# Kernel tuning notes

Hardware: AMD Instinct MI355X
Metric: run time of the kernel (lower is better)

Reference implementation:

```python
import jax, jax.numpy as jnp
import numpy as np

B, FIXED_LEN, N_FRAME, MID, P = 4096, 8192, 2112, 264, 88
UNROLLED_ITER = 5


def setup_inputs() -> dict:
    key = jax.random.key(0)
    ks = jax.random.split(key, 8)
    # Fourier weights scaled by 1/FIXED_LEN as in fourier_init
    W_cos = jax.random.normal(ks[0], (N_FRAME, FIXED_LEN), jnp.float32) / FIXED_LEN
    W_sin = jax.random.normal(ks[1], (N_FRAME, FIXED_LEN), jnp.float32) / FIXED_LEN
    # template is |cisoid_dict|^2 >= 0; small positive values keep the unrolled loop stable
    template = jax.random.uniform(ks[2], (N_FRAME, MID), jnp.float32) * 0.01
    return {
        "input_this": jax.random.normal(ks[3], (B, FIXED_LEN), jnp.float32),
        "input_prev": jax.random.normal(ks[4], (B, FIXED_LEN), jnp.float32),
        "W_cos": W_cos,
        "W_sin": W_sin,
        "template": template,
        "W1": jax.random.normal(ks[5], (MID, MID), jnp.float32) * 0.05 + jnp.eye(MID, dtype=jnp.float32),
        "b1": jnp.zeros((MID,), jnp.float32),
        "W2": jax.random.normal(ks[6], (P, MID), jnp.float32) * 0.1,
        "b2": jnp.zeros((P,), jnp.float32),
        "Wout": jax.random.normal(ks[7], (P, P), jnp.float32) * 0.1 + 4.0 * jnp.eye(P, dtype=jnp.float32),
        "bout": jnp.full((P,), -3.0, jnp.float32),
    }


def reference(input_this, input_prev, W_cos, W_sin, template, W1, b1, W2, b2, Wout, bout):
    fixed_len = jnp.asarray(input_this.shape[1], input_this.dtype)
    # get_feat: normalized power spectrum features
    n_valid = (jnp.count_nonzero(input_this, axis=1) + 1).astype(input_this.dtype)[:, None]
    scale = fixed_len / n_valid                      # [B, 1]
    x_cos = (input_this @ W_cos.T) * scale           # [B, N_FRAME]
    x_sin = (input_this @ W_sin.T) * scale
    feat = x_cos * x_cos + x_sin * x_sin             # [B, N_FRAME]

    # process_feat: unrolled LISTA-style iterations
    running = feat
    xi = -running
    m = jax.nn.relu(-10.0 * (xi @ template))         # [B, MID]
    for _ in range(UNROLLED_ITER - 1):
        xi = 1.6 * ((m @ template.T) - running) + 0.2 * xi
        m = jax.nn.relu(-8.0 * (xi @ template) + 0.2 * m)

    h = jax.nn.relu(jax.nn.relu(m @ W1.T + b1) @ W2.T + b2)  # [B, P]
    return jax.nn.sigmoid(h @ Wout.T + bout)         # velocity_estimate [B, P]
```

## Files before the change

kernel.cpp:

```cpp
#include <hip/hip_runtime.h>
#include <cstdint>
#include <cstddef>

#define B_SZ 4096
#define KLEN 8192
#define NF   2112
#define MID  264
#define PD   88

typedef _Float16 f16;
typedef _Float16 f16x4 __attribute__((ext_vector_type(4)));
typedef _Float16 f16x8 __attribute__((ext_vector_type(8)));
typedef float    f32x4 __attribute__((ext_vector_type(4)));

__device__ __forceinline__ void gl2lds16(const void* g, void* l) {
    __builtin_amdgcn_global_load_lds(
        (const __attribute__((address_space(1))) void*)g,
        (__attribute__((address_space(3))) void*)l, 16, 0, 0);
}

__global__ void k_row_prep(const float* __restrict__ x, f16* __restrict__ xh,
                           float* __restrict__ alpha) {
    const int row = blockIdx.x;
    const float* xr = x + (size_t)row * KLEN;
    f16* xhr = xh + (size_t)row * KLEN;
    int cnt = 0;
    for (int j = threadIdx.x * 4; j < KLEN; j += 256 * 4) {
        float4 v = *(const float4*)(xr + j);
        f16x4 h = { (f16)v.x, (f16)v.y, (f16)v.z, (f16)v.w };
        *(f16x4*)(xhr + j) = h;
        cnt += (v.x != 0.f) + (v.y != 0.f) + (v.z != 0.f) + (v.w != 0.f);
    }
    for (int off = 32; off > 0; off >>= 1) cnt += __shfl_down(cnt, off);
    __shared__ int lsum[4];
    if ((threadIdx.x & 63) == 0) lsum[threadIdx.x >> 6] = cnt;
    __syncthreads();
    if (threadIdx.x == 0)
        alpha[row] = 8.0f / (float)(lsum[0] + lsum[1] + lsum[2] + lsum[3] + 1);
}

__global__ void k_cvt_w2(const float* __restrict__ wc, const float* __restrict__ ws,
                         f16* __restrict__ whc, f16* __restrict__ whs, int n4) {
    const float* w = blockIdx.y ? ws : wc;
    f16* wh = blockIdx.y ? whs : whc;
    for (int i = blockIdx.x * blockDim.x + threadIdx.x; i < n4; i += gridDim.x * blockDim.x) {
        float4 v = ((const float4*)w)[i];
        f16x4 h = { (f16)(v.x * 8192.f), (f16)(v.y * 8192.f),
                    (f16)(v.z * 8192.f), (f16)(v.w * 8192.f) };
        ((f16x4*)wh)[i] = h;
    }
}

__global__ void k_prep_tt(const float* __restrict__ T, f16* __restrict__ tt) {
    __shared__ float tile[32][33];
    const int k0 = blockIdx.x * 32, n0 = blockIdx.y * 32;
    const int tx = threadIdx.x & 31, ty = threadIdx.x >> 5;
    for (int r = ty; r < 32; r += 8) {
        const int k = k0 + r, n = n0 + tx;
        tile[r][tx] = (n < MID) ? T[(size_t)k * MID + n] : 0.f;
    }
    __syncthreads();
    for (int r = ty; r < 32; r += 8) {
        const int n = n0 + r, k = k0 + tx;
        tt[(size_t)n * NF + k] = (f16)tile[tx][r];
    }
}

__global__ void k_gram(const float* __restrict__ T, float* __restrict__ G) {
    __shared__ float Pp[32][64];
    __shared__ float Qq[32][64];
    const int i0 = blockIdx.x * 64, j0 = blockIdx.y * 64;
    const int tx = threadIdx.x & 15, ty = threadIdx.x >> 4;
    float acc[4][4] = {};
    for (int kc = blockIdx.z * 11; kc < (int)blockIdx.z * 11 + 11; ++kc) {
        const int k0 = kc * 32;
        for (int l = threadIdx.x; l < 32 * 64; l += 256) {
            const int kk = l >> 6, cc = l & 63, kr = k0 + kk;
            Pp[kk][cc] = (i0 + cc < MID) ? T[(size_t)kr * MID + i0 + cc] : 0.f;
            Qq[kk][cc] = (j0 + cc < MID) ? T[(size_t)kr * MID + j0 + cc] : 0.f;
        }
        __syncthreads();
        for (int kk = 0; kk < 32; ++kk) {
            float a_[4], b_[4];
#pragma unroll
            for (int u = 0; u < 4; ++u) a_[u] = Pp[kk][tx * 4 + u];
#pragma unroll
            for (int w = 0; w < 4; ++w) b_[w] = Qq[kk][ty * 4 + w];
#pragma unroll
            for (int u = 0; u < 4; ++u)
#pragma unroll
                for (int w = 0; w < 4; ++w) acc[u][w] += a_[u] * b_[w];
        }
        __syncthreads();
    }
    for (int u = 0; u < 4; ++u) {
        const int gi = i0 + tx * 4 + u;
        if (gi >= MID) continue;
        for (int w = 0; w < 4; ++w) {
            const int gj = j0 + ty * 4 + w;
            if (gj < MID) atomicAdd(&G[(size_t)gi * MID + gj], acc[u][w]);
        }
    }
}

__global__ __launch_bounds__(256, 4) void k_fourier(
    const f16* __restrict__ A, const f16* __restrict__ Bc, const f16* __restrict__ Bs,
    const float* __restrict__ alpha, f16* __restrict__ feat) {
    __shared__ __align__(16) f16 As[128 * 64];
    __shared__ __align__(16) f16 Bcs[64 * 64];
    __shared__ __align__(16) f16 Bss[64 * 64];
    const int tid = threadIdx.x, lane = tid & 63, wave = tid >> 6;
    const int wm = wave & 1, wn = wave >> 1;

    const int bid = blockIdx.y * 33 + blockIdx.x;
    const int swz = (bid & 7) * 132 + (bid >> 3);
    const int bx = swz % 33, by = swz / 33;
    const int m0 = by * 128, n0 = bx * 64;

    const int srow = tid >> 3;
    const int scol = ((tid & 7) ^ (srow & 7)) << 3;
    const f16* gA  = A  + (size_t)(m0 + srow) * KLEN + scol;
    const f16* gBc = Bc + (size_t)(n0 + srow) * KLEN + scol;
    const f16* gBs = Bs + (size_t)(n0 + srow) * KLEN + scol;

#define STAGE_F(kq)                                                               \
    {                                                                             \
        _Pragma("unroll")                                                         \
        for (int i = 0; i < 4; ++i)                                               \
            gl2lds16(gA + (size_t)(32 * i) * KLEN + (kq),                         \
                     (char*)&As[0] + (tid + 256 * i) * 16);                       \
        _Pragma("unroll")                                                         \
        for (int i = 0; i < 2; ++i)                                               \
            gl2lds16(gBc + (size_t)(32 * i) * KLEN + (kq),                        \
                     (char*)&Bcs[0] + (tid + 256 * i) * 16);                      \
        _Pragma("unroll")                                                         \
        for (int i = 0; i < 2; ++i)                                               \
            gl2lds16(gBs + (size_t)(32 * i) * KLEN + (kq),                        \
                     (char*)&Bss[0] + (tid + 256 * i) * 16);                      \
    }

    f32x4 accC[4][2], accS[4][2];
    const f32x4 z4 = {0.f, 0.f, 0.f, 0.f};
#pragma unroll
    for (int i = 0; i < 4; ++i)
#pragma unroll
        for (int j = 0; j < 2; ++j) { accC[i][j] = z4; accS[i][j] = z4; }

    for (int k0 = 0; k0 < KLEN; k0 += 64) {
        if (k0) __syncthreads();
        STAGE_F(k0);
        __syncthreads();
#pragma unroll
        for (int kk = 0; kk < 2; ++kk) {
            const int chunk0 = kk * 4 + (lane >> 4);
            f16x8 af[4], bcf[2], bsf[2];
#pragma unroll
            for (int mt = 0; mt < 4; ++mt) {
                const int r = wm * 64 + mt * 16 + (lane & 15);
                af[mt] = *(const f16x8*)(&As[0] + r * 64 + ((chunk0 ^ (r & 7)) << 3));
            }
#pragma unroll
            for (int nt = 0; nt < 2; ++nt) {
                const int r = wn * 32 + nt * 16 + (lane & 15);
                const int off = r * 64 + ((chunk0 ^ (r & 7)) << 3);
                bcf[nt] = *(const f16x8*)(&Bcs[0] + off);
                bsf[nt] = *(const f16x8*)(&Bss[0] + off);
            }
#pragma unroll
            for (int mt = 0; mt < 4; ++mt)
#pragma unroll
                for (int nt = 0; nt < 2; ++nt) {
                    accC[mt][nt] = __builtin_amdgcn_mfma_f32_16x16x32_f16(af[mt], bcf[nt], accC[mt][nt], 0, 0, 0);
                    accS[mt][nt] = __builtin_amdgcn_mfma_f32_16x16x32_f16(af[mt], bsf[nt], accS[mt][nt], 0, 0, 0);
                }
        }
    }
#undef STAGE_F
#pragma unroll
    for (int mt = 0; mt < 4; ++mt)
#pragma unroll
        for (int reg = 0; reg < 4; ++reg) {
            const int row = m0 + wm * 64 + mt * 16 + ((lane >> 4) << 2) + reg;
            const float al = alpha[row];
#pragma unroll
            for (int nt = 0; nt < 2; ++nt) {
                const int col = n0 + wn * 32 + nt * 16 + (lane & 15);
                const float xc = accC[mt][nt][reg] * al;
                const float xs = accS[mt][nt][reg] * al;
                feat[(size_t)row * NF + col] = (f16)(xc * xc + xs * xs);
            }
        }
}

__global__ __launch_bounds__(256, 2) void k_ggemm(
    const f16* __restrict__ A, const f16* __restrict__ Bt, float* __restrict__ g64) {
    __shared__ __align__(16) f16 As[2][128 * 64];
    __shared__ __align__(16) f16 Bs_[2][64 * 64];
    const int tid = threadIdx.x, lane = tid & 63, wave = tid >> 6;
    const int wm = wave & 1, wn = wave >> 1;
    const int m0 = blockIdx.y * 128, n0 = blockIdx.x * 64;
    const int srow = tid >> 3;
    const int scol = ((tid & 7) ^ (srow & 7)) << 3;
    const f16* gA = A + (size_t)(m0 + srow) * NF + scol;
    const f16* gB = Bt + (size_t)(n0 + srow) * NF + scol;

#define STAGE_G(buf, kq)                                                          \
    {                                                                             \
        _Pragma("unroll")                                                         \
        for (int i = 0; i < 4; ++i)                                               \
            gl2lds16(gA + (size_t)(32 * i) * NF + (kq),                           \
                     (char*)&As[buf][0] + (tid + 256 * i) * 16);                  \
        _Pragma("unroll")                                                         \
        for (int i = 0; i < 2; ++i)                                               \
            gl2lds16(gB + (size_t)(32 * i) * NF + (kq),                           \
                     (char*)&Bs_[buf][0] + (tid + 256 * i) * 16);                 \
    }

    f32x4 acc[4][2];
    const f32x4 z4 = {0.f, 0.f, 0.f, 0.f};
#pragma unroll
    for (int i = 0; i < 4; ++i)
#pragma unroll
        for (int j = 0; j < 2; ++j) acc[i][j] = z4;

    STAGE_G(0, 0);
    for (int k0 = 0; k0 < NF; k0 += 64) {
        const int cur = (k0 >> 6) & 1;
        __syncthreads();
        if (k0 + 64 < NF) STAGE_G(cur ^ 1, k0 + 64);
#pragma unroll
        for (int kk = 0; kk < 2; ++kk) {
            const int chunk0 = kk * 4 + (lane >> 4);
            f16x8 af[4], bf[2];
#pragma unroll
            for (int mt = 0; mt < 4; ++mt) {
                const int r = wm * 64 + mt * 16 + (lane & 15);
                af[mt] = *(const f16x8*)(&As[cur][0] + r * 64 + ((chunk0 ^ (r & 7)) << 3));
            }
#pragma unroll
            for (int nt = 0; nt < 2; ++nt) {
                const int r = wn * 32 + nt * 16 + (lane & 15);
                bf[nt] = *(const f16x8*)(&Bs_[cur][0] + r * 64 + ((chunk0 ^ (r & 7)) << 3));
            }
#pragma unroll
            for (int mt = 0; mt < 4; ++mt)
#pragma unroll
                for (int nt = 0; nt < 2; ++nt)
                    acc[mt][nt] = __builtin_amdgcn_mfma_f32_16x16x32_f16(af[mt], bf[nt], acc[mt][nt], 0, 0, 0);
        }
    }
#undef STAGE_G
#pragma unroll
    for (int mt = 0; mt < 4; ++mt)
#pragma unroll
        for (int reg = 0; reg < 4; ++reg) {
            const int row = m0 + wm * 64 + mt * 16 + ((lane >> 4) << 2) + reg;
#pragma unroll
            for (int nt = 0; nt < 2; ++nt) {
                const int col = n0 + wn * 32 + nt * 16 + (lane & 15);
                if (col < MID) g64[(size_t)row * MID + col] = acc[mt][nt][reg];
            }
        }
}

__global__ __launch_bounds__(320) void k_tail(
    const float* __restrict__ g64, const float* __restrict__ Gm,
    const float* __restrict__ W1, const float* __restrict__ b1,
    const float* __restrict__ W2, const float* __restrict__ b2,
    const float* __restrict__ Wout, const float* __restrict__ bout,
    float* __restrict__ out) {
    __shared__ __align__(16) float m_l[8 * 268];
    __shared__ __align__(16) float h2_l[8 * 92];
    const int t = threadIdx.x;
    const int r0 = blockIdx.x * 8;
    const bool act = (t < 264);
    const int rb = (t & 3) * 2;
    const int cb = (t >> 2) * 4;

    for (int idx = t; idx < 8 * MID; idx += 320) {
        const int r = idx / MID, c = idx - r * MID;
        const float gv = g64[(size_t)r0 * MID + idx] * 0.015625f;
        m_l[r * 268 + c] = fmaxf(10.f * gv, 0.f);
    }
    float gr[2][4], ur[2][4];
    if (act) {
#pragma unroll
        for (int u = 0; u < 2; ++u) {
            const float4 gq = *(const float4*)&g64[(size_t)(r0 + rb + u) * MID + cb];
            gr[u][0] = gq.x * 0.015625f; gr[u][1] = gq.y * 0.015625f;
            gr[u][2] = gq.z * 0.015625f; gr[u][3] = gq.w * 0.015625f;
#pragma unroll
            for (int j = 0; j < 4; ++j) ur[u][j] = -gr[u][j];
        }
    }
    __syncthreads();

    for (int it = 0; it < 4; ++it) {
        float v[2][4];
        if (act) {
#pragma unroll
            for (int u = 0; u < 2; ++u)
#pragma unroll
                for (int j = 0; j < 4; ++j) v[u][j] = 0.f;
            for (int k = 0; k < MID; k += 4) {
                float4 m4[2];
#pragma unroll
                for (int u = 0; u < 2; ++u) m4[u] = *(const float4*)&m_l[(rb + u) * 268 + k];
#pragma unroll
                for (int j = 0; j < 4; ++j) {
                    const float4 gv4 = *(const float4*)&Gm[(size_t)(cb + j) * MID + k];
#pragma unroll
                    for (int u = 0; u < 2; ++u)
                        v[u][j] += m4[u].x * gv4.x + m4[u].y * gv4.y + m4[u].z * gv4.z + m4[u].w * gv4.w;
                }
            }
        }
        __syncthreads();
        if (act) {
#pragma unroll
            for (int u = 0; u < 2; ++u)
#pragma unroll
                for (int j = 0; j < 4; ++j) {
                    const float un = 1.6f * (v[u][j] - gr[u][j]) + 0.2f * ur[u][j];
                    ur[u][j] = un;
                    float* mp = &m_l[(rb + u) * 268 + cb + j];
                    *mp = fmaxf(-8.f * un + 0.2f * (*mp), 0.f);
                }
        }
        __syncthreads();
    }

    {
        float v[2][4];
        if (act) {
#pragma unroll
            for (int u = 0; u < 2; ++u)
#pragma unroll
                for (int j = 0; j < 4; ++j) v[u][j] = 0.f;
            for (int k = 0; k < MID; k += 4) {
                float4 m4[2];
#pragma unroll
                for (int u = 0; u < 2; ++u) m4[u] = *(const float4*)&m_l[(rb + u) * 268 + k];
#pragma unroll
                for (int j = 0; j < 4; ++j) {
                    const float4 wv = *(const float4*)&W1[(size_t)(cb + j) * MID + k];
#pragma unroll
                    for (int u = 0; u < 2; ++u)
                        v[u][j] += m4[u].x * wv.x + m4[u].y * wv.y + m4[u].z * wv.z + m4[u].w * wv.w;
                }
            }
        }
        __syncthreads();
        if (act) {
#pragma unroll
            for (int u = 0; u < 2; ++u)
#pragma unroll
                for (int j = 0; j < 4; ++j)
                    m_l[(rb + u) * 268 + cb + j] = fmaxf(v[u][j] + b1[cb + j], 0.f);
        }
        __syncthreads();
    }

    const bool act2 = (t < 88);
    const int rb2 = (t & 3) * 2, cb2 = (t >> 2) * 4;
    if (act2) {
        float v[2][4];
#pragma unroll
        for (int u = 0; u < 2; ++u)
#pragma unroll
            for (int j = 0; j < 4; ++j) v[u][j] = 0.f;
        for (int k = 0; k < MID; k += 4) {
            float4 m4[2];
#pragma unroll
            for (int u = 0; u < 2; ++u) m4[u] = *(const float4*)&m_l[(rb2 + u) * 268 + k];
#pragma unroll
            for (int j = 0; j < 4; ++j) {
                const float4 wv = *(const float4*)&W2[(size_t)(cb2 + j) * MID + k];
#pragma unroll
                for (int u = 0; u < 2; ++u)
                    v[u][j] += m4[u].x * wv.x + m4[u].y * wv.y + m4[u].z * wv.z + m4[u].w * wv.w;
            }
        }
#pragma unroll
        for (int u = 0; u < 2; ++u)
#pragma unroll
            for (int j = 0; j < 4; ++j)
                h2_l[(rb2 + u) * 92 + cb2 + j] = fmaxf(v[u][j] + b2[cb2 + j], 0.f);
    }
    __syncthreads();
    if (act2) {
        float v[2][4];
#pragma unroll
        for (int u = 0; u < 2; ++u)
#pragma unroll
            for (int j = 0; j < 4; ++j) v[u][j] = 0.f;
        for (int q = 0; q < PD; q += 4) {
            float4 h4[2];
#pragma unroll
            for (int u = 0; u < 2; ++u) h4[u] = *(const float4*)&h2_l[(rb2 + u) * 92 + q];
#pragma unroll
            for (int j = 0; j < 4; ++j) {
                const float4 wv = *(const float4*)&Wout[(size_t)(cb2 + j) * PD + q];
#pragma unroll
                for (int u = 0; u < 2; ++u)
                    v[u][j] += h4[u].x * wv.x + h4[u].y * wv.y + h4[u].z * wv.z + h4[u].w * wv.w;
            }
        }
#pragma unroll
        for (int u = 0; u < 2; ++u) {
            float4 o;
            o.x = 1.f / (1.f + expf(-(v[u][0] + bout[cb2 + 0])));
            o.y = 1.f / (1.f + expf(-(v[u][1] + bout[cb2 + 1])));
            o.z = 1.f / (1.f + expf(-(v[u][2] + bout[cb2 + 2])));
            o.w = 1.f / (1.f + expf(-(v[u][3] + bout[cb2 + 3])));
            *(float4*)&out[(size_t)(r0 + rb2 + u) * PD + cb2] = o;
        }
    }
}

extern "C" void kernel_launch(void* const* d_in, const int* in_sizes, int n_in,
                              void* d_out, int out_size, void* d_ws, size_t ws_size,
                              hipStream_t stream) {
    (void)in_sizes; (void)n_in; (void)out_size; (void)ws_size;
    const float* inp  = (const float*)d_in[0];
    const float* wcos = (const float*)d_in[2];
    const float* wsin = (const float*)d_in[3];
    const float* tmpl = (const float*)d_in[4];
    const float* W1   = (const float*)d_in[5];
    const float* b1   = (const float*)d_in[6];
    const float* W2   = (const float*)d_in[7];
    const float* b2   = (const float*)d_in[8];
    const float* Wout = (const float*)d_in[9];
    const float* bout = (const float*)d_in[10];
    float* out = (float*)d_out;

    char* p = (char*)d_ws;
    f16* a_h    = (f16*)p;   p += (size_t)B_SZ * KLEN * 2;
    f16* wc_h   = (f16*)p;   p += (size_t)NF * KLEN * 2;
    f16* ws_h   = (f16*)p;   p += (size_t)NF * KLEN * 2;
    f16* feat_h = (f16*)p;   p += (size_t)B_SZ * NF * 2;
    f16* tt_h   = (f16*)p;   p += (size_t)320 * NF * 2;
    float* alpha= (float*)p; p += (size_t)B_SZ * 4;
    float* g64  = (float*)p; p += (size_t)B_SZ * MID * 4;
    float* Gm   = (float*)p; p += (size_t)MID * MID * 4;

    hipMemsetAsync(Gm, 0, (size_t)MID * MID * 4, stream);
    k_row_prep<<<B_SZ, 256, 0, stream>>>(inp, a_h, alpha);
    k_cvt_w2<<<dim3(2048, 2), 256, 0, stream>>>(wcos, wsin, wc_h, ws_h,
                                                (int)((size_t)NF * KLEN / 4));
    k_prep_tt<<<dim3(NF / 32, 10), 256, 0, stream>>>(tmpl, tt_h);
    k_gram<<<dim3(5, 5, 6), 256, 0, stream>>>(tmpl, Gm);
    k_fourier<<<dim3(NF / 64, B_SZ / 128), 256, 0, stream>>>(a_h, wc_h, ws_h, alpha, feat_h);
    k_ggemm<<<dim3(5, B_SZ / 128), 256, 0, stream>>>(feat_h, tt_h, g64);
    k_tail<<<B_SZ / 8, 320, 0, stream>>>(g64, Gm, W1, b1, W2, b2, Wout, bout, out);
}
```

Before: 958.4 us.

## Add four-stage LDS ring buffer pipeline to Fourier GEMM kernel

Splits the Fourier GEMM K loop into 32-wide slices held in a four-deep LDS ring buffer. Direct global-to-LDS loads are issued three stages ahead and gated by vmcnt waits and a single barrier per stage, so memory latency overlaps with MFMA work. The change also raises MFMA issue priority with s_setprio and reworks the XOR swizzle for the narrower tiles. Launch bounds drop from 4 to 2 blocks per SU because LDS use per block grows, which costs occupancy.

```diff
diff --git a/kernel.cpp b/kernel.cpp
--- a/kernel.cpp
+++ b/kernel.cpp
@@ -103,12 +103,12 @@
     }
 }
 
-__global__ __launch_bounds__(256, 4) void k_fourier(
+__global__ __launch_bounds__(256, 2) void k_fourier(
     const f16* __restrict__ A, const f16* __restrict__ Bc, const f16* __restrict__ Bs,
     const float* __restrict__ alpha, f16* __restrict__ feat) {
-    __shared__ __align__(16) f16 As[128 * 64];
-    __shared__ __align__(16) f16 Bcs[64 * 64];
-    __shared__ __align__(16) f16 Bss[64 * 64];
+    __shared__ __align__(16) f16 As4[4][128 * 32];
+    __shared__ __align__(16) f16 Bcs4[4][64 * 32];
+    __shared__ __align__(16) f16 Bss4[4][64 * 32];
     const int tid = threadIdx.x, lane = tid & 63, wave = tid >> 6;
     const int wm = wave & 1, wn = wave >> 1;
 
@@ -117,26 +117,32 @@
     const int bx = swz % 33, by = swz / 33;
     const int m0 = by * 128, n0 = bx * 64;
 
-    const int srow = tid >> 3;
-    const int scol = ((tid & 7) ^ (srow & 7)) << 3;
-    const f16* gA  = A  + (size_t)(m0 + srow) * KLEN + scol;
-    const f16* gBc = Bc + (size_t)(n0 + srow) * KLEN + scol;
-    const f16* gBs = Bs + (size_t)(n0 + srow) * KLEN + scol;
-
-#define STAGE_F(kq)                                                               \
+    const int srow = tid >> 2;
+    const int cswz = ((tid & 3) ^ ((tid >> 3) & 3)) << 3;
+    const f16* pA  = A  + (size_t)(m0 + srow) * KLEN + cswz;
+    const f16* pBc = Bc + (size_t)(n0 + srow) * KLEN + cswz;
+    const f16* pBs = Bs + (size_t)(n0 + srow) * KLEN + cswz;
+
+#define STAGE_F(h, b)                                                             \
     {                                                                             \
-        _Pragma("unroll")                                                         \
-        for (int i = 0; i < 4; ++i)                                               \
-            gl2lds16(gA + (size_t)(32 * i) * KLEN + (kq),                         \
-                     (char*)&As[0] + (tid + 256 * i) * 16);                       \
-        _Pragma("unroll")                                                         \
-        for (int i = 0; i < 2; ++i)                                               \
-            gl2lds16(gBc + (size_t)(32 * i) * KLEN + (kq),                        \
-                     (char*)&Bcs[0] + (tid + 256 * i) * 16);                      \
-        _Pragma("unroll")                                                         \
-        for (int i = 0; i < 2; ++i)                                               \
-            gl2lds16(gBs + (size_t)(32 * i) * KLEN + (kq),                        \
-                     (char*)&Bss[0] + (tid + 256 * i) * 16);                      \
+        gl2lds16(pA + (size_t)(h) * 32, (char*)&As4[b][0] + tid * 16);            \
+        gl2lds16(pA + (size_t)64 * KLEN + (size_t)(h) * 32,                       \
+                 (char*)&As4[b][0] + (tid + 256) * 16);                           \
+        gl2lds16(pBc + (size_t)(h) * 32, (char*)&Bcs4[b][0] + tid * 16);          \
+        gl2lds16(pBs + (size_t)(h) * 32, (char*)&Bss4[b][0] + tid * 16);          \
+    }
+
+    const int c0 = lane >> 4;
+    int offA[4], offB[2];
+#pragma unroll
+    for (int mt = 0; mt < 4; ++mt) {
+        const int r = wm * 64 + mt * 16 + (lane & 15);
+        offA[mt] = r * 32 + ((c0 ^ ((r >> 1) & 3)) << 3);
+    }
+#pragma unroll
+    for (int nt = 0; nt < 2; ++nt) {
+        const int r = wn * 32 + nt * 16 + (lane & 15);
+        offB[nt] = r * 32 + ((c0 ^ ((r >> 1) & 3)) << 3);
     }
 
     f32x4 accC[4][2], accS[4][2];
@@ -146,36 +152,52 @@
 #pragma unroll
         for (int j = 0; j < 2; ++j) { accC[i][j] = z4; accS[i][j] = z4; }
 
-    for (int k0 = 0; k0 < KLEN; k0 += 64) {
-        if (k0) __syncthreads();
-        STAGE_F(k0);
-        __syncthreads();
-#pragma unroll
-        for (int kk = 0; kk < 2; ++kk) {
-            const int chunk0 = kk * 4 + (lane >> 4);
-            f16x8 af[4], bcf[2], bsf[2];
-#pragma unroll
-            for (int mt = 0; mt < 4; ++mt) {
-                const int r = wm * 64 + mt * 16 + (lane & 15);
-                af[mt] = *(const f16x8*)(&As[0] + r * 64 + ((chunk0 ^ (r & 7)) << 3));
-            }
-#pragma unroll
-            for (int nt = 0; nt < 2; ++nt) {
-                const int r = wn * 32 + nt * 16 + (lane & 15);
-                const int off = r * 64 + ((chunk0 ^ (r & 7)) << 3);
-                bcf[nt] = *(const f16x8*)(&Bcs[0] + off);
-                bsf[nt] = *(const f16x8*)(&Bss[0] + off);
-            }
-#pragma unroll
-            for (int mt = 0; mt < 4; ++mt)
-#pragma unroll
-                for (int nt = 0; nt < 2; ++nt) {
-                    accC[mt][nt] = __builtin_amdgcn_mfma_f32_16x16x32_f16(af[mt], bcf[nt], accC[mt][nt], 0, 0, 0);
-                    accS[mt][nt] = __builtin_amdgcn_mfma_f32_16x16x32_f16(af[mt], bsf[nt], accS[mt][nt], 0, 0, 0);
-                }
-        }
-    }
+#define COMPUTE_F(b)                                                              \
+    {                                                                             \
+        f16x8 af[4], bcf[2], bsf[2];                                              \
+        _Pragma("unroll")                                                         \
+        for (int mt = 0; mt < 4; ++mt)                                            \
+            af[mt] = *(const f16x8*)(&As4[b][offA[mt]]);                          \
+        _Pragma("unroll")                                                         \
+        for (int nt = 0; nt < 2; ++nt) {                                          \
+            bcf[nt] = *(const f16x8*)(&Bcs4[b][offB[nt]]);                        \
+            bsf[nt] = *(const f16x8*)(&Bss4[b][offB[nt]]);                        \
+        }                                                                         \
+        __builtin_amdgcn_s_setprio(1);                                            \
+        _Pragma("unroll")                                                         \
+        for (int mt = 0; mt < 4; ++mt)                                            \
+            _Pragma("unroll")                                                     \
+            for (int nt = 0; nt < 2; ++nt) {                                      \
+                accC[mt][nt] = __builtin_amdgcn_mfma_f32_16x16x32_f16(            \
+                    af[mt], bcf[nt], accC[mt][nt], 0, 0, 0);                      \
+                accS[mt][nt] = __builtin_amdgcn_mfma_f32_16x16x32_f16(            \
+                    af[mt], bsf[nt], accS[mt][nt], 0, 0, 0);                      \
+            }                                                                     \
+        __builtin_amdgcn_s_setprio(0);                                            \
+    }
+
+#define WAITB(n)                                                                  \
+    asm volatile("s_waitcnt vmcnt(" #n ")" ::: "memory");                         \
+    __builtin_amdgcn_s_barrier();
+
+    STAGE_F(0, 0); STAGE_F(1, 1); STAGE_F(2, 2);
+    WAITB(8);
+
+#pragma unroll 1
+    for (int h = 0; h < 252; h += 4) {
+        STAGE_F(h + 3, 3); COMPUTE_F(0); WAITB(8);
+        STAGE_F(h + 4, 0); COMPUTE_F(1); WAITB(8);
+        STAGE_F(h + 5, 1); COMPUTE_F(2); WAITB(8);
+        STAGE_F(h + 6, 2); COMPUTE_F(3); WAITB(8);
+    }
+    STAGE_F(255, 3); COMPUTE_F(0); WAITB(8);
+    COMPUTE_F(1); WAITB(4);
+    COMPUTE_F(2); WAITB(0);
+    COMPUTE_F(3);
 #undef STAGE_F
+#undef COMPUTE_F
+#undef WAITB
+
 #pragma unroll
     for (int mt = 0; mt < 4; ++mt)
 #pragma unroll
```

After: 1.098 ms. 14.5% more time.
